# Performance work log

Measured on AMD Instinct MI355X. Metric: run time of the kernel, lower is better.

Reference implementation:

```python
import jax, jax.numpy as jnp
import numpy as np

N_NODES = 50000


def gcn_conv(x, edge_index, W, b, num_nodes):
    """PyG GCNConv: add self-loops, symmetric norm, gather-scatter aggregate."""
    h = x @ W  # [N, out]
    row = jnp.concatenate([edge_index[0], jnp.arange(num_nodes)])  # sources (+ self loops)
    col = jnp.concatenate([edge_index[1], jnp.arange(num_nodes)])  # targets
    deg = jax.ops.segment_sum(jnp.ones_like(col, dtype=h.dtype), col, num_segments=num_nodes)
    dinv = jnp.where(deg > 0, jax.lax.rsqrt(deg), 0.0)
    norm = dinv[row] * dinv[col]  # [E+N]
    msgs = h[row] * norm[:, None]  # gather + scale
    out = jax.ops.segment_sum(msgs, col, num_segments=num_nodes)  # scatter-add
    return out + b


def setup_inputs() -> dict:
    key = jax.random.key(0)
    ks = jax.random.split(key, 8)
    F_in, H, D = 50, 50, 64
    E_train, Ep, En = 1600000, 200000, 200000
    x = jax.random.normal(ks[0], (N_NODES, F_in), dtype=jnp.float32)
    train_pos_edge_index = jax.random.randint(ks[1], (2, E_train), 0, N_NODES)
    pos_edge_index = jax.random.randint(ks[2], (2, Ep), 0, N_NODES)
    neg_edge_index = jax.random.randint(ks[3], (2, En), 0, N_NODES)
    # Glorot-ish params for the two GCN layers
    W1 = jax.random.normal(ks[4], (F_in, H), dtype=jnp.float32) * (1.0 / np.sqrt(F_in))
    b1 = jnp.zeros((H,), dtype=jnp.float32)
    W2 = jax.random.normal(ks[5], (H, D), dtype=jnp.float32) * (1.0 / np.sqrt(H))
    b2 = jnp.zeros((D,), dtype=jnp.float32)
    return {"x": x, "train_pos_edge_index": train_pos_edge_index,
            "pos_edge_index": pos_edge_index, "neg_edge_index": neg_edge_index,
            "W1": W1, "b1": b1, "W2": W2, "b2": b2}


def reference(x, train_pos_edge_index, pos_edge_index, neg_edge_index, W1, b1, W2, b2):
    # encode: conv1 -> relu -> conv2
    h = gcn_conv(x, train_pos_edge_index, W1, b1, N_NODES)
    h = jax.nn.relu(h)
    z = gcn_conv(h, train_pos_edge_index, W2, b2, N_NODES)  # [N, D]
    # decode: dot product over concatenated pos/neg edge endpoints
    edge_index = jnp.concatenate([pos_edge_index, neg_edge_index], axis=-1)
    logits = jnp.sum(z[edge_index[0]] * z[edge_index[1]], axis=-1)  # [Ep+En]
    return logits
```

## Files before the change

kernel.cpp:

```cpp
#include <hip/hip_runtime.h>
#include <hip/hip_bf16.h>
#include <hip/hip_fp16.h>


constexpr int N_NODES = 50000;
constexpr int NBITS = 6;
constexpr int BNODES = 1 << NBITS;
constexpr int NBUCK = (N_NODES + BNODES - 1) / BNODES;
constexpr int CAP = 2560;
constexpr int CHUNK = 6144;
constexpr int NTILE = 8;
constexpr int TROWS = 6250;

union H4 {
    uint2 u;
    __half2 h[2];
};

__device__ inline float4 h4_to_f4(H4 a) {
    float2 f0 = __half22float2(a.h[0]);
    float2 f1 = __half22float2(a.h[1]);
    return make_float4(f0.x, f0.y, f1.x, f1.y);
}

__device__ inline H4 f4_to_h4(float4 v) {
    H4 r;
    r.h[0] = __floats2half2_rn(v.x, v.y);
    r.h[1] = __floats2half2_rn(v.z, v.w);
    return r;
}

__device__ inline void unpack16(uint4 w0, uint4 w1, int* r) {
    r[0] = (int)(w0.x & 0xffffu);  r[1] = (int)(w0.x >> 16);
    r[2] = (int)(w0.y & 0xffffu);  r[3] = (int)(w0.y >> 16);
    r[4] = (int)(w0.z & 0xffffu);  r[5] = (int)(w0.z >> 16);
    r[6] = (int)(w0.w & 0xffffu);  r[7] = (int)(w0.w >> 16);
    r[8] = (int)(w1.x & 0xffffu);  r[9] = (int)(w1.x >> 16);
    r[10] = (int)(w1.y & 0xffffu); r[11] = (int)(w1.y >> 16);
    r[12] = (int)(w1.z & 0xffffu); r[13] = (int)(w1.z >> 16);
    r[14] = (int)(w1.w & 0xffffu); r[15] = (int)(w1.w >> 16);
}

__device__ inline float hdot2(unsigned ua, unsigned ub) {
    __half2 ha = *(__half2*)&ua;
    __half2 hb = *(__half2*)&ub;
    float2 fa = __half22float2(ha);
    float2 fb = __half22float2(hb);
    return fa.x * fb.x + fa.y * fb.y;
}

__global__ __launch_bounds__(256) void partition_kernel(const int4* __restrict__ row4,
                                                        const int4* __restrict__ col4, int E,
                                                        int* __restrict__ cursor,
                                                        unsigned* __restrict__ bEdges) {
    __shared__ unsigned ed[CHUNK];
    __shared__ int cnt[NBUCK];
    __shared__ int base[NBUCK];
    int t = threadIdx.x;
    int e0 = blockIdx.x * CHUNK;
    int n = min(CHUNK, E - e0);
    int n4 = n >> 2;
    for (int i = t; i < NBUCK; i += 256) cnt[i] = 0;
    __syncthreads();
    const int4* r4 = row4 + (e0 >> 2);
    const int4* c4 = col4 + (e0 >> 2);
    for (int i = t; i < n4; i += 256) {
        int4 r = r4[i];
        int4 c = c4[i];
        ed[i * 4 + 0] = ((unsigned)r.x << 16) | (unsigned)c.x;
        ed[i * 4 + 1] = ((unsigned)r.y << 16) | (unsigned)c.y;
        ed[i * 4 + 2] = ((unsigned)r.z << 16) | (unsigned)c.z;
        ed[i * 4 + 3] = ((unsigned)r.w << 16) | (unsigned)c.w;
        atomicAdd(&cnt[c.x >> NBITS], 1);
        atomicAdd(&cnt[c.y >> NBITS], 1);
        atomicAdd(&cnt[c.z >> NBITS], 1);
        atomicAdd(&cnt[c.w >> NBITS], 1);
    }
    __syncthreads();
    for (int i = t; i < NBUCK; i += 256) base[i] = cnt[i] ? atomicAdd(&cursor[i], cnt[i]) : 0;
    __syncthreads();
    for (int i = t; i < NBUCK; i += 256) cnt[i] = 0;
    __syncthreads();
    for (int i = t; i < n; i += 256) {
        unsigned p = ed[i];
        int bk = (int)(p & 0xffffu) >> NBITS;
        int pos = base[bk] + atomicAdd(&cnt[bk], 1);
        if (pos < CAP) bEdges[(size_t)bk * CAP + pos] = p;
    }
}

__global__ __launch_bounds__(256) void bucket_csr_mm_kernel(const int* __restrict__ cursor,
                                                            const unsigned* __restrict__ bEdges,
                                                            const float* __restrict__ x,
                                                            const float* __restrict__ W1,
                                                            unsigned short* __restrict__ srcIdx,
                                                            unsigned* __restrict__ rowmeta,
                                                            float* __restrict__ dinv,
                                                            uint2* __restrict__ Hs, int N) {
    __shared__ unsigned ed[CAP];
    __shared__ unsigned short srcL[CAP];
    __shared__ int tdeg[BNODES * NTILE];
    __shared__ int toff[BNODES * NTILE];
    __shared__ int totPad;
    __shared__ float dinvL[BNODES];
    __shared__ float4 Ws4[50 * 16];
    __shared__ float xs[BNODES][51];
    int b = blockIdx.x;
    int tx = threadIdx.x;
    int cnt = min(cursor[b], CAP);
    for (int i = tx; i < BNODES * NTILE; i += 256) tdeg[i] = 0;
    for (int i = tx; i < CAP; i += 256) srcL[i] = 0;
    __syncthreads();
    const unsigned* seg = bEdges + (size_t)b * CAP;
    for (int i = tx; i < cnt; i += 256) {
        unsigned p = seg[i];
        ed[i] = p;
        int l = p & (BNODES - 1);
        int tl = (int)(p >> 16) / TROWS;
        atomicAdd(&tdeg[l * NTILE + tl], 1);
    }
    for (int i = tx; i < 50 * 64; i += 256) {
        int k = i >> 6;
        int c = i & 63;
        ((float*)Ws4)[i] = (c < 50) ? W1[k * 50 + c] : 0.f;
    }
    for (int i = tx; i < BNODES * 50; i += 256) {
        int l = i / 50;
        int k = i - l * 50;
        int node = b * BNODES + l;
        xs[l][k] = (node < N) ? x[(size_t)node * 50 + k] : 0.f;
    }
    __syncthreads();
    if (tx < BNODES) {
        int sd[NTILE];
        int d = 0;
#pragma unroll
        for (int u = 0; u < NTILE; ++u) {
            sd[u] = tdeg[tx * NTILE + u];
            d += sd[u];
        }
        int dpad = (d + 7) & ~7;
        int s = dpad;
#pragma unroll
        for (int off = 1; off < BNODES; off <<= 1) {
            int o = __shfl_up(s, off, 64);
            if (tx >= off) s += o;
        }
        int ex = s - dpad;
        int run = ex;
#pragma unroll
        for (int u = 0; u < NTILE; ++u) {
            toff[tx * NTILE + u] = run;
            run += sd[u];
        }
        if (tx == 63) totPad = min(s, CAP);
        float dvv = rsqrtf((float)d + 1.0f);
        dinvL[tx] = dvv;
        int node = b * BNODES + tx;
        if (node < N) {
            unsigned st = (unsigned)(b * CAP + ex);
            rowmeta[node] = (st << 7) | (unsigned)d;
            dinv[node] = dvv;
        }
    }
    __syncthreads();
    for (int i = tx; i < BNODES * NTILE; i += 256) tdeg[i] = 0;
    __syncthreads();
    for (int i = tx; i < cnt; i += 256) {
        unsigned p = ed[i];
        int l = p & (BNODES - 1);
        int tl = (int)(p >> 16) / TROWS;
        int pos = toff[l * NTILE + tl] + atomicAdd(&tdeg[l * NTILE + tl], 1);
        srcL[pos] = (unsigned short)(p >> 16);
    }
    __syncthreads();
    int tot = totPad;
    for (int i = tx; i < tot; i += 256) srcIdx[(size_t)b * CAP + i] = srcL[i];
    int q = tx & 15;
    int g = tx >> 4;
#pragma unroll
    for (int rep = 0; rep < 4; ++rep) {
        int l = g + rep * 16;
        float4 acc = make_float4(0.f, 0.f, 0.f, 0.f);
#pragma unroll
        for (int k = 0; k < 50; ++k) {
            float xv = xs[l][k];
            float4 w = Ws4[k * 16 + q];
            acc.x = fmaf(xv, w.x, acc.x);
            acc.y = fmaf(xv, w.y, acc.y);
            acc.z = fmaf(xv, w.z, acc.z);
            acc.w = fmaf(xv, w.w, acc.w);
        }
        float dv = dinvL[l];
        acc.x *= dv;
        acc.y *= dv;
        acc.z *= dv;
        acc.w *= dv;
        int node = b * BNODES + l;
        if (node < N) Hs[(size_t)node * 16 + q] = f4_to_h4(acc).u;
    }
}

__device__ inline float4 gather_sum(const unsigned short* __restrict__ srcIdx,
                                    const uint2* __restrict__ hs, int node, int q,
                                    unsigned meta) {
    int start = (int)(meta >> 7);
    int d = (int)(meta & 127u);
    int end = start + d;
    H4 t;
    t.u = hs[(size_t)node * 16 + q];
    float4 acc = h4_to_f4(t);
    int j = start;
    while (j + 16 <= end) {
        const uint4* ip = (const uint4*)(srcIdx + j);
        int r[16];
        unpack16(ip[0], ip[1], r);
#pragma unroll
        for (int u = 0; u < 16; ++u) {
            H4 hv;
            hv.u = hs[(size_t)r[u] * 16 + q];
            float4 a = h4_to_f4(hv);
            acc.x += a.x;
            acc.y += a.y;
            acc.z += a.z;
            acc.w += a.w;
        }
        j += 16;
    }
    if (j < end) {
        const uint4* ip = (const uint4*)(srcIdx + j);
        int r[16];
        unpack16(ip[0], ip[1], r);
#pragma unroll
        for (int u = 0; u < 16; ++u) {
            float m = (j + u < end) ? 1.f : 0.f;
            H4 hv;
            hv.u = hs[(size_t)r[u] * 16 + q];
            float4 a = h4_to_f4(hv);
            acc.x = fmaf(m, a.x, acc.x);
            acc.y = fmaf(m, a.y, acc.y);
            acc.z = fmaf(m, a.z, acc.z);
            acc.w = fmaf(m, a.w, acc.w);
        }
    }
    return acc;
}

template <int BC>
__global__ __launch_bounds__(256) void agg_mm_kernel(const unsigned* __restrict__ rowmeta,
                                                     const unsigned short* __restrict__ srcIdx,
                                                     const uint2* __restrict__ hs,
                                                     const float* __restrict__ dinv,
                                                     const float* __restrict__ b1,
                                                     const float* __restrict__ W2,
                                                     uint2* __restrict__ out, int N) {
    __shared__ float4 Ws4[50 * 16];
    __shared__ float h1s[16][68];
    for (int i = threadIdx.x; i < 50 * 64; i += 256) ((float*)Ws4)[i] = W2[i];
    __syncthreads();
    int tid = blockIdx.x * blockDim.x + threadIdx.x;
    int node = tid >> 4;
    int q = tid & 15;
    int g = threadIdx.x >> 4;
    float4 acc = gather_sum(srcIdx, hs, node, q, rowmeta[node]);
    float dv = dinv[node];
    int f = q * 4;
    float4 h1;
    h1.x = fmaxf(dv * acc.x + (f + 0 < BC ? b1[f + 0] : 0.f), 0.f);
    h1.y = fmaxf(dv * acc.y + (f + 1 < BC ? b1[f + 1] : 0.f), 0.f);
    h1.z = fmaxf(dv * acc.z + (f + 2 < BC ? b1[f + 2] : 0.f), 0.f);
    h1.w = fmaxf(dv * acc.w + (f + 3 < BC ? b1[f + 3] : 0.f), 0.f);
    h1s[g][f + 0] = h1.x;
    h1s[g][f + 1] = h1.y;
    h1s[g][f + 2] = h1.z;
    h1s[g][f + 3] = h1.w;
    __syncthreads();
    float4 a2 = make_float4(0.f, 0.f, 0.f, 0.f);
#pragma unroll
    for (int k = 0; k < 50; ++k) {
        float xv = h1s[g][k];
        float4 w = Ws4[k * 16 + q];
        a2.x = fmaf(xv, w.x, a2.x);
        a2.y = fmaf(xv, w.y, a2.y);
        a2.z = fmaf(xv, w.z, a2.z);
        a2.w = fmaf(xv, w.w, a2.w);
    }
    a2.x *= dv;
    a2.y *= dv;
    a2.z *= dv;
    a2.w *= dv;
    out[(size_t)node * 16 + q] = f4_to_h4(a2).u;
}

template <int BC>
__global__ __launch_bounds__(256) void agg_kernel(const unsigned* __restrict__ rowmeta,
                                                  const unsigned short* __restrict__ srcIdx,
                                                  const uint2* __restrict__ hs,
                                                  const float* __restrict__ dinv,
                                                  const float* __restrict__ b,
                                                  uint2* __restrict__ out, int N) {
    int tid = blockIdx.x * blockDim.x + threadIdx.x;
    int node = tid >> 4;
    int q = tid & 15;
    if (node >= N) return;
    float4 acc = gather_sum(srcIdx, hs, node, q, rowmeta[node]);
    float dv = dinv[node];
    int f = q * 4;
    float4 v;
    v.x = dv * acc.x + (f + 0 < BC ? b[f + 0] : 0.f);
    v.y = dv * acc.y + (f + 1 < BC ? b[f + 1] : 0.f);
    v.z = dv * acc.z + (f + 2 < BC ? b[f + 2] : 0.f);
    v.w = dv * acc.w + (f + 3 < BC ? b[f + 3] : 0.f);
    out[(size_t)node * 16 + q] = f4_to_h4(v).u;
}

__global__ __launch_bounds__(256) void decode_kernel(const int* __restrict__ pos,
                                                     const int* __restrict__ neg, int Ep, int En,
                                                     const uint4* __restrict__ z4,
                                                     float* __restrict__ logits) {
    int tid = blockIdx.x * blockDim.x + threadIdx.x;
    int e = tid >> 3;
    int q = tid & 7;
    int Etot = Ep + En;
    if (e >= Etot) return;
    int a, bn;
    if (e < Ep) {
        a = pos[e];
        bn = pos[Ep + e];
    } else {
        int t = e - Ep;
        a = neg[t];
        bn = neg[En + t];
    }
    uint4 ua = z4[(size_t)a * 8 + q];
    uint4 ub = z4[(size_t)bn * 8 + q];
    float v = hdot2(ua.x, ub.x) + hdot2(ua.y, ub.y) + hdot2(ua.z, ub.z) + hdot2(ua.w, ub.w);
    v += __shfl_xor(v, 1, 64);
    v += __shfl_xor(v, 2, 64);
    v += __shfl_xor(v, 4, 64);
    if (q == 0) logits[e] = v;
}

extern "C" void kernel_launch(void* const* d_in, const int* in_sizes, int n_in,
                              void* d_out, int out_size, void* d_ws, size_t ws_size,
                              hipStream_t stream) {
    const float* x = (const float*)d_in[0];
    const int* train = (const int*)d_in[1];
    const int* pos = (const int*)d_in[2];
    const int* neg = (const int*)d_in[3];
    const float* W1 = (const float*)d_in[4];
    const float* b1 = (const float*)d_in[5];
    const float* W2 = (const float*)d_in[6];
    const float* b2 = (const float*)d_in[7];
    float* logits = (float*)d_out;

    const int FIN = 50;
    const int N = in_sizes[0] / FIN;
    const int E = in_sizes[1] / 2;
    const int Ep = in_sizes[2] / 2;
    const int En = in_sizes[3] / 2;

    const int* t_row = train;
    const int* t_col = train + E;

    float* dinv = (float*)d_ws;
    __half* buf0 = (__half*)(dinv + N);
    __half* buf1 = buf0 + (size_t)N * 64;
    unsigned* rowmeta = (unsigned*)(buf1 + (size_t)N * 64);
    int* cursor = (int*)(rowmeta + N);
    uintptr_t sp = (uintptr_t)(cursor + NBUCK);
    sp = (sp + 15) & ~(uintptr_t)15;
    unsigned short* srcIdx = (unsigned short*)sp;
    uintptr_t bp = (uintptr_t)(srcIdx + (size_t)NBUCK * CAP);
    bp = (bp + 15) & ~(uintptr_t)15;
    unsigned* bEdges = (unsigned*)bp;

    hipMemsetAsync(cursor, 0, (size_t)NBUCK * sizeof(int), stream);

    partition_kernel<<<(E + CHUNK - 1) / CHUNK, 256, 0, stream>>>((const int4*)t_row,
                                                                  (const int4*)t_col, E, cursor,
                                                                  bEdges);
    bucket_csr_mm_kernel<<<NBUCK, 256, 0, stream>>>(cursor, bEdges, x, W1, srcIdx, rowmeta, dinv,
                                                    (uint2*)buf0, N);

    const int MMB = (N * 16 + 255) / 256;

    agg_mm_kernel<50><<<MMB, 256, 0, stream>>>(rowmeta, srcIdx, (const uint2*)buf0, dinv, b1, W2,
                                               (uint2*)buf1, N);
    agg_kernel<64><<<MMB, 256, 0, stream>>>(rowmeta, srcIdx, (const uint2*)buf1, dinv, b2,
                                            (uint2*)buf0, N);
    decode_kernel<<<((Ep + En) * 8 + 255) / 256, 256, 0, stream>>>(pos, neg, Ep, En,
                                                                   (const uint4*)buf0, logits);
}
```

Baseline: 216.1 us.

## Widen aggregation gathers to 16-byte loads with 8 threads per node

The two aggregation kernels now assign 8 lanes per node, each loading 16 bytes (8 halves) per neighbour instead of 4 halves with 16 lanes. In the first layer the eighth lane skips its gather entirely, since only 50 of the 64 features are real. This is meant to halve the number of gather instructions and lanes per edge and drop useless padding loads. The index unrolling goes from 16 to 8 per iteration, and the partition kernel is launched with 512 threads. Register pressure grows per thread, and the agg_mm kernel drops the barrier after loading the weights into shared memory, relying on the later barrier to cover it.

```diff
diff --git a/kernel.cpp b/kernel.cpp
--- a/kernel.cpp
+++ b/kernel.cpp
@@ -9,6 +9,7 @@
 constexpr int NBUCK = (N_NODES + BNODES - 1) / BNODES;
 constexpr int CAP = 2560;
 constexpr int CHUNK = 6144;
+constexpr int PTHREADS = 512;
 constexpr int NTILE = 8;
 constexpr int TROWS = 6250;
 
@@ -17,11 +18,10 @@
     __half2 h[2];
 };
 
-__device__ inline float4 h4_to_f4(H4 a) {
-    float2 f0 = __half22float2(a.h[0]);
-    float2 f1 = __half22float2(a.h[1]);
-    return make_float4(f0.x, f0.y, f1.x, f1.y);
-}
+union H8 {
+    uint4 u;
+    __half2 h[4];
+};
 
 __device__ inline H4 f4_to_h4(float4 v) {
     H4 r;
@@ -30,15 +30,40 @@
     return r;
 }
 
-__device__ inline void unpack16(uint4 w0, uint4 w1, int* r) {
-    r[0] = (int)(w0.x & 0xffffu);  r[1] = (int)(w0.x >> 16);
-    r[2] = (int)(w0.y & 0xffffu);  r[3] = (int)(w0.y >> 16);
-    r[4] = (int)(w0.z & 0xffffu);  r[5] = (int)(w0.z >> 16);
-    r[6] = (int)(w0.w & 0xffffu);  r[7] = (int)(w0.w >> 16);
-    r[8] = (int)(w1.x & 0xffffu);  r[9] = (int)(w1.x >> 16);
-    r[10] = (int)(w1.y & 0xffffu); r[11] = (int)(w1.y >> 16);
-    r[12] = (int)(w1.z & 0xffffu); r[13] = (int)(w1.z >> 16);
-    r[14] = (int)(w1.w & 0xffffu); r[15] = (int)(w1.w >> 16);
+__device__ inline uint4 pack8(float4 A, float4 B) {
+    H8 r;
+    r.h[0] = __floats2half2_rn(A.x, A.y);
+    r.h[1] = __floats2half2_rn(A.z, A.w);
+    r.h[2] = __floats2half2_rn(B.x, B.y);
+    r.h[3] = __floats2half2_rn(B.z, B.w);
+    return r.u;
+}
+
+__device__ inline void unpack8(uint4 w, int* r) {
+    r[0] = (int)(w.x & 0xffffu);  r[1] = (int)(w.x >> 16);
+    r[2] = (int)(w.y & 0xffffu);  r[3] = (int)(w.y >> 16);
+    r[4] = (int)(w.z & 0xffffu);  r[5] = (int)(w.z >> 16);
+    r[6] = (int)(w.w & 0xffffu);  r[7] = (int)(w.w >> 16);
+}
+
+__device__ inline void add8(float4& A, float4& B, H8 v) {
+    float2 g0 = __half22float2(v.h[0]);
+    float2 g1 = __half22float2(v.h[1]);
+    float2 g2 = __half22float2(v.h[2]);
+    float2 g3 = __half22float2(v.h[3]);
+    A.x += g0.x; A.y += g0.y; A.z += g1.x; A.w += g1.y;
+    B.x += g2.x; B.y += g2.y; B.z += g3.x; B.w += g3.y;
+}
+
+__device__ inline void fma8(float4& A, float4& B, H8 v, float m) {
+    float2 g0 = __half22float2(v.h[0]);
+    float2 g1 = __half22float2(v.h[1]);
+    float2 g2 = __half22float2(v.h[2]);
+    float2 g3 = __half22float2(v.h[3]);
+    A.x = fmaf(m, g0.x, A.x); A.y = fmaf(m, g0.y, A.y);
+    A.z = fmaf(m, g1.x, A.z); A.w = fmaf(m, g1.y, A.w);
+    B.x = fmaf(m, g2.x, B.x); B.y = fmaf(m, g2.y, B.y);
+    B.z = fmaf(m, g3.x, B.z); B.w = fmaf(m, g3.y, B.w);
 }
 
 __device__ inline float hdot2(unsigned ua, unsigned ub) {
@@ -49,10 +74,10 @@
     return fa.x * fb.x + fa.y * fb.y;
 }
 
-__global__ __launch_bounds__(256) void partition_kernel(const int4* __restrict__ row4,
-                                                        const int4* __restrict__ col4, int E,
-                                                        int* __restrict__ cursor,
-                                                        unsigned* __restrict__ bEdges) {
+__global__ __launch_bounds__(PTHREADS) void partition_kernel(const int4* __restrict__ row4,
+                                                             const int4* __restrict__ col4, int E,
+                                                             int* __restrict__ cursor,
+                                                             unsigned* __restrict__ bEdges) {
     __shared__ unsigned ed[CHUNK];
     __shared__ int cnt[NBUCK];
     __shared__ int base[NBUCK];
@@ -60,11 +85,11 @@
     int e0 = blockIdx.x * CHUNK;
     int n = min(CHUNK, E - e0);
     int n4 = n >> 2;
-    for (int i = t; i < NBUCK; i += 256) cnt[i] = 0;
+    for (int i = t; i < NBUCK; i += PTHREADS) cnt[i] = 0;
     __syncthreads();
     const int4* r4 = row4 + (e0 >> 2);
     const int4* c4 = col4 + (e0 >> 2);
-    for (int i = t; i < n4; i += 256) {
+    for (int i = t; i < n4; i += PTHREADS) {
         int4 r = r4[i];
         int4 c = c4[i];
         ed[i * 4 + 0] = ((unsigned)r.x << 16) | (unsigned)c.x;
@@ -77,11 +102,11 @@
         atomicAdd(&cnt[c.w >> NBITS], 1);
     }
     __syncthreads();
-    for (int i = t; i < NBUCK; i += 256) base[i] = cnt[i] ? atomicAdd(&cursor[i], cnt[i]) : 0;
-    __syncthreads();
-    for (int i = t; i < NBUCK; i += 256) cnt[i] = 0;
-    __syncthreads();
-    for (int i = t; i < n; i += 256) {
+    for (int i = t; i < NBUCK; i += PTHREADS) base[i] = cnt[i] ? atomicAdd(&cursor[i], cnt[i]) : 0;
+    __syncthreads();
+    for (int i = t; i < NBUCK; i += PTHREADS) cnt[i] = 0;
+    __syncthreads();
+    for (int i = t; i < n; i += PTHREADS) {
         unsigned p = ed[i];
         int bk = (int)(p & 0xffffu) >> NBITS;
         int pos = base[bk] + atomicAdd(&cnt[bk], 1);
@@ -201,117 +226,117 @@
     }
 }
 
-__device__ inline float4 gather_sum(const unsigned short* __restrict__ srcIdx,
-                                    const uint2* __restrict__ hs, int node, int q,
-                                    unsigned meta) {
+__device__ inline void gather_sum8(const unsigned short* __restrict__ srcIdx,
+                                   const uint4* __restrict__ hs, int node, int q,
+                                   unsigned meta, float4& A, float4& B) {
     int start = (int)(meta >> 7);
     int d = (int)(meta & 127u);
     int end = start + d;
-    H4 t;
-    t.u = hs[(size_t)node * 16 + q];
-    float4 acc = h4_to_f4(t);
+    H8 t;
+    t.u = hs[(size_t)node * 8 + q];
+    {
+        float2 g0 = __half22float2(t.h[0]);
+        float2 g1 = __half22float2(t.h[1]);
+        float2 g2 = __half22float2(t.h[2]);
+        float2 g3 = __half22float2(t.h[3]);
+        A = make_float4(g0.x, g0.y, g1.x, g1.y);
+        B = make_float4(g2.x, g2.y, g3.x, g3.y);
+    }
     int j = start;
-    while (j + 16 <= end) {
-        const uint4* ip = (const uint4*)(srcIdx + j);
-        int r[16];
-        unpack16(ip[0], ip[1], r);
-#pragma unroll
-        for (int u = 0; u < 16; ++u) {
-            H4 hv;
-            hv.u = hs[(size_t)r[u] * 16 + q];
-            float4 a = h4_to_f4(hv);
-            acc.x += a.x;
-            acc.y += a.y;
-            acc.z += a.z;
-            acc.w += a.w;
-        }
-        j += 16;
+    while (j + 8 <= end) {
+        uint4 w = *(const uint4*)(srcIdx + j);
+        int r[8];
+        unpack8(w, r);
+#pragma unroll
+        for (int u = 0; u < 8; ++u) {
+            H8 hv;
+            hv.u = hs[(size_t)r[u] * 8 + q];
+            add8(A, B, hv);
+        }
+        j += 8;
     }
     if (j < end) {
-        const uint4* ip = (const uint4*)(srcIdx + j);
-        int r[16];
-        unpack16(ip[0], ip[1], r);
-#pragma unroll
-        for (int u = 0; u < 16; ++u) {
+        uint4 w = *(const uint4*)(srcIdx + j);
+        int r[8];
+        unpack8(w, r);
+#pragma unroll
+        for (int u = 0; u < 8; ++u) {
             float m = (j + u < end) ? 1.f : 0.f;
-            H4 hv;
-            hv.u = hs[(size_t)r[u] * 16 + q];
-            float4 a = h4_to_f4(hv);
-            acc.x = fmaf(m, a.x, acc.x);
-            acc.y = fmaf(m, a.y, acc.y);
-            acc.z = fmaf(m, a.z, acc.z);
-            acc.w = fmaf(m, a.w, acc.w);
-        }
-    }
-    return acc;
+            H8 hv;
+            hv.u = hs[(size_t)r[u] * 8 + q];
+            fma8(A, B, hv, m);
+        }
+    }
 }
 
 template <int BC>
 __global__ __launch_bounds__(256) void agg_mm_kernel(const unsigned* __restrict__ rowmeta,
                                                      const unsigned short* __restrict__ srcIdx,
-                                                     const uint2* __restrict__ hs,
+                                                     const uint4* __restrict__ hs,
                                                      const float* __restrict__ dinv,
                                                      const float* __restrict__ b1,
                                                      const float* __restrict__ W2,
-                                                     uint2* __restrict__ out, int N) {
+                                                     uint4* __restrict__ out, int N) {
     __shared__ float4 Ws4[50 * 16];
-    __shared__ float h1s[16][68];
+    __shared__ float h1s[32][68];
     for (int i = threadIdx.x; i < 50 * 64; i += 256) ((float*)Ws4)[i] = W2[i];
-    __syncthreads();
     int tid = blockIdx.x * blockDim.x + threadIdx.x;
-    int node = tid >> 4;
-    int q = tid & 15;
-    int g = threadIdx.x >> 4;
-    float4 acc = gather_sum(srcIdx, hs, node, q, rowmeta[node]);
-    float dv = dinv[node];
-    int f = q * 4;
-    float4 h1;
-    h1.x = fmaxf(dv * acc.x + (f + 0 < BC ? b1[f + 0] : 0.f), 0.f);
-    h1.y = fmaxf(dv * acc.y + (f + 1 < BC ? b1[f + 1] : 0.f), 0.f);
-    h1.z = fmaxf(dv * acc.z + (f + 2 < BC ? b1[f + 2] : 0.f), 0.f);
-    h1.w = fmaxf(dv * acc.w + (f + 3 < BC ? b1[f + 3] : 0.f), 0.f);
-    h1s[g][f + 0] = h1.x;
-    h1s[g][f + 1] = h1.y;
-    h1s[g][f + 2] = h1.z;
-    h1s[g][f + 3] = h1.w;
-    __syncthreads();
-    float4 a2 = make_float4(0.f, 0.f, 0.f, 0.f);
+    int node = tid >> 3;
+    int q = tid & 7;
+    int g = threadIdx.x >> 3;
+    int nodeC = min(node, N - 1);
+    float4 A = make_float4(0.f, 0.f, 0.f, 0.f), B = A;
+    if (q < 7) gather_sum8(srcIdx, hs, nodeC, q, rowmeta[nodeC], A, B);
+    float dv = dinv[nodeC];
+    int f = q * 8;
+    float hv[8] = {A.x, A.y, A.z, A.w, B.x, B.y, B.z, B.w};
+#pragma unroll
+    for (int u = 0; u < 8; ++u) {
+        float bb = (f + u < BC) ? b1[f + u] : 0.f;
+        h1s[g][f + u] = fmaxf(dv * hv[u] + bb, 0.f);
+    }
+    __syncthreads();
+    float4 aA = make_float4(0.f, 0.f, 0.f, 0.f), aB = aA;
 #pragma unroll
     for (int k = 0; k < 50; ++k) {
         float xv = h1s[g][k];
-        float4 w = Ws4[k * 16 + q];
-        a2.x = fmaf(xv, w.x, a2.x);
-        a2.y = fmaf(xv, w.y, a2.y);
-        a2.z = fmaf(xv, w.z, a2.z);
-        a2.w = fmaf(xv, w.w, a2.w);
-    }
-    a2.x *= dv;
-    a2.y *= dv;
-    a2.z *= dv;
-    a2.w *= dv;
-    out[(size_t)node * 16 + q] = f4_to_h4(a2).u;
+        float4 wA = Ws4[k * 16 + 2 * q];
+        float4 wB = Ws4[k * 16 + 2 * q + 1];
+        aA.x = fmaf(xv, wA.x, aA.x);
+        aA.y = fmaf(xv, wA.y, aA.y);
+        aA.z = fmaf(xv, wA.z, aA.z);
+        aA.w = fmaf(xv, wA.w, aA.w);
+        aB.x = fmaf(xv, wB.x, aB.x);
+        aB.y = fmaf(xv, wB.y, aB.y);
+        aB.z = fmaf(xv, wB.z, aB.z);
+        aB.w = fmaf(xv, wB.w, aB.w);
+    }
+    aA.x *= dv; aA.y *= dv; aA.z *= dv; aA.w *= dv;
+    aB.x *= dv; aB.y *= dv; aB.z *= dv; aB.w *= dv;
+    if (node < N) out[(size_t)node * 8 + q] = pack8(aA, aB);
 }
 
 template <int BC>
 __global__ __launch_bounds__(256) void agg_kernel(const unsigned* __restrict__ rowmeta,
                                                   const unsigned short* __restrict__ srcIdx,
-                                                  const uint2* __restrict__ hs,
+                                                  const uint4* __restrict__ hs,
                                                   const float* __restrict__ dinv,
                                                   const float* __restrict__ b,
-                                                  uint2* __restrict__ out, int N) {
+                                                  uint4* __restrict__ out, int N) {
     int tid = blockIdx.x * blockDim.x + threadIdx.x;
-    int node = tid >> 4;
-    int q = tid & 15;
+    int node = tid >> 3;
+    int q = tid & 7;
     if (node >= N) return;
-    float4 acc = gather_sum(srcIdx, hs, node, q, rowmeta[node]);
+    float4 A, B;
+    gather_sum8(srcIdx, hs, node, q, rowmeta[node], A, B);
     float dv = dinv[node];
-    int f = q * 4;
-    float4 v;
-    v.x = dv * acc.x + (f + 0 < BC ? b[f + 0] : 0.f);
-    v.y = dv * acc.y + (f + 1 < BC ? b[f + 1] : 0.f);
-    v.z = dv * acc.z + (f + 2 < BC ? b[f + 2] : 0.f);
-    v.w = dv * acc.w + (f + 3 < BC ? b[f + 3] : 0.f);
-    out[(size_t)node * 16 + q] = f4_to_h4(v).u;
+    int f = q * 8;
+    float hv[8] = {A.x, A.y, A.z, A.w, B.x, B.y, B.z, B.w};
+    float o[8];
+#pragma unroll
+    for (int u = 0; u < 8; ++u) o[u] = dv * hv[u] + (f + u < BC ? b[f + u] : 0.f);
+    out[(size_t)node * 8 + q] =
+        pack8(make_float4(o[0], o[1], o[2], o[3]), make_float4(o[4], o[5], o[6], o[7]));
 }
 
 __global__ __launch_bounds__(256) void decode_kernel(const int* __restrict__ pos,
@@ -377,18 +402,18 @@
 
     hipMemsetAsync(cursor, 0, (size_t)NBUCK * sizeof(int), stream);
 
-    partition_kernel<<<(E + CHUNK - 1) / CHUNK, 256, 0, stream>>>((const int4*)t_row,
-                                                                  (const int4*)t_col, E, cursor,
-                                                                  bEdges);
+    partition_kernel<<<(E + CHUNK - 1) / CHUNK, PTHREADS, 0, stream>>>((const int4*)t_row,
+                                                                       (const int4*)t_col, E,
+                                                                       cursor, bEdges);
     bucket_csr_mm_kernel<<<NBUCK, 256, 0, stream>>>(cursor, bEdges, x, W1, srcIdx, rowmeta, dinv,
                                                     (uint2*)buf0, N);
 
-    const int MMB = (N * 16 + 255) / 256;
-
-    agg_mm_kernel<50><<<MMB, 256, 0, stream>>>(rowmeta, srcIdx, (const uint2*)buf0, dinv, b1, W2,
-                                               (uint2*)buf1, N);
-    agg_kernel<64><<<MMB, 256, 0, stream>>>(rowmeta, srcIdx, (const uint2*)buf1, dinv, b2,
-                                            (uint2*)buf0, N);
+    const int AGB = (N * 8 + 255) / 256;
+
+    agg_mm_kernel<50><<<AGB, 256, 0, stream>>>(rowmeta, srcIdx, (const uint4*)buf0, dinv, b1, W2,
+                                               (uint4*)buf1, N);
+    agg_kernel<64><<<AGB, 256, 0, stream>>>(rowmeta, srcIdx, (const uint4*)buf1, dinv, b2,
+                                            (uint4*)buf0, N);
     decode_kernel<<<((Ep + En) * 8 + 255) / 256, 256, 0, stream>>>(pos, neg, Ep, En,
                                                                    (const uint4*)buf0, logits);
 }
```

After: 212.4 us. Within noise of the previous version (-1.7%).
